# Performance work log

Hardware: AMD Instinct MI355X
Metric: run time of the kernel (lower is better)

The kernel has to match this reference:

```python
import jax, jax.numpy as jnp
import numpy as np

E = 8        # n_experts
K = 2        # top-k
DIM = 1024
HID = 2048   # swiglu hidden; fc1 out = 2*HID
B, T = 4, 2048


def setup_inputs() -> dict:
    key = jax.random.key(0)
    ks = jax.random.split(key, 7)
    s = 0.02
    return {
        "x": jax.random.normal(ks[0], (B, T, DIM), dtype=jnp.float32),
        "router_w": jax.random.normal(ks[1], (E, DIM), dtype=jnp.float32) * s,
        "router_b": jnp.zeros((E,), dtype=jnp.float32),
        "W1": jax.random.normal(ks[2], (E, DIM, 2 * HID), dtype=jnp.float32) * s,
        "b1": jnp.zeros((E, 2 * HID), dtype=jnp.float32),
        "W2": jax.random.normal(ks[3], (E, HID, DIM), dtype=jnp.float32) * s,
        "b2": jnp.zeros((E, DIM), dtype=jnp.float32),
    }


def _swiglu(h):
    h1, h2 = jnp.split(h, 2, axis=-1)
    return jax.nn.silu(h1) * h2


def reference(x, router_w, router_b, W1, b1, W2, b2):
    # Router: logits = Linear(dim, E), temperature = 1.0
    logits = jnp.einsum("btd,ed->bte", x, router_w) + router_b  # [B,T,E]
    topk_val, topk_idx = jax.lax.top_k(logits, K)               # [B,T,K]
    weights = jax.nn.softmax(topk_val, axis=-1)                 # softmax router
    # combine[b,t,e] = sum_k weights[b,t,k] * [topk_idx[b,t,k] == e]
    combine = jnp.sum(jax.nn.one_hot(topk_idx, E, dtype=x.dtype)
                      * weights[..., None], axis=-2)            # [B,T,E]
    out = jnp.zeros_like(x)
    # Fixed small loop over experts (structurally distinct weight slices).
    for e in range(E):
        h = jnp.einsum("btd,dh->bth", x, W1[e]) + b1[e]         # [B,T,2H]
        y = jnp.einsum("bth,hd->btd", _swiglu(h), W2[e]) + b2[e]
        out = out + combine[..., e:e + 1] * y
    return out
```

## Files before the change

### kernel.cpp

```cpp
#include <hip/hip_runtime.h>
#include <stdint.h>

typedef unsigned short u16;

#define E_    8
#define DIM_  1024
#define HID_  2048
#define H2_   4096
#define NTOK  8192

typedef __attribute__((ext_vector_type(8))) short bf16x8;
typedef __attribute__((ext_vector_type(4))) float f32x4;

__device__ __forceinline__ u16 f2bf(float f) {
  uint32_t u = __builtin_bit_cast(uint32_t, f);
  uint32_t r = (u + 0x7FFFu + ((u >> 16) & 1u)) >> 16;
  return (u16)r;
}
__device__ __forceinline__ float bf2f(u16 u) {
  return __builtin_bit_cast(float, (uint32_t)u << 16);
}

__device__ __forceinline__ void gload16(const void* g, void* l) {
  __builtin_amdgcn_global_load_lds(
      (const __attribute__((address_space(1))) void*)g,
      (__attribute__((address_space(3))) void*)l, 16, 0, 0);
}


__global__ void tconv(const float* __restrict__ src, u16* __restrict__ dst, int R, int C) {
  __shared__ float t[64][65];
  int e = blockIdx.z;
  int r0 = blockIdx.y * 64, c0 = blockIdx.x * 64;
  const float* s = src + (size_t)e * R * C;
  u16* d = dst + (size_t)e * R * C;
  int tid = threadIdx.x;
  int rr = tid >> 4, cc = (tid & 15) * 4;
#pragma unroll
  for (int p = 0; p < 4; ++p) {
    float4 v = *(const float4*)(s + (size_t)(r0 + p * 16 + rr) * C + c0 + cc);
    t[p * 16 + rr][cc + 0] = v.x; t[p * 16 + rr][cc + 1] = v.y;
    t[p * 16 + rr][cc + 2] = v.z; t[p * 16 + rr][cc + 3] = v.w;
  }
  __syncthreads();
  int cr = tid >> 3, rc = (tid & 7) * 8;
#pragma unroll
  for (int p = 0; p < 2; ++p) {
    union { u16 u[8]; uint4 v; } w;
#pragma unroll
    for (int j = 0; j < 8; ++j) w.u[j] = f2bf(t[rc + j][p * 32 + cr]);
    *(uint4*)(d + (size_t)(c0 + p * 32 + cr) * R + r0 + rc) = w.v;
  }
}


__global__ void routerA(const float* __restrict__ x, const float* __restrict__ rw,
                        const float* __restrict__ rb, u16* __restrict__ xb,
                        int* __restrict__ gcnt, int2* __restrict__ te_l,
                        float2* __restrict__ tw) {
  __shared__ float srw[E_ * DIM_];
  __shared__ float sb[E_];
  __shared__ int   hcnt[E_];

  int tid = threadIdx.x;
  for (int i = tid; i < E_ * DIM_ / 4; i += 256)
    ((float4*)srw)[i] = ((const float4*)rw)[i];
  if (tid < E_) { sb[tid] = rb[tid]; hcnt[tid] = 0; }
  __syncthreads();

  int wid = tid >> 6, lane = tid & 63;
#pragma unroll
  for (int s = 0; s < 2; ++s) {
    int t = blockIdx.x * 8 + wid * 2 + s;
    const float* xt = x + (size_t)t * DIM_;
    float acc[8] = {0.f, 0.f, 0.f, 0.f, 0.f, 0.f, 0.f, 0.f};
#pragma unroll
    for (int it = 0; it < 4; ++it) {
      int d = it * 256 + lane * 4;
      float4 xv = *(const float4*)(xt + d);
      ushort4 xo;
      xo.x = f2bf(xv.x); xo.y = f2bf(xv.y); xo.z = f2bf(xv.z); xo.w = f2bf(xv.w);
      *(ushort4*)(xb + (size_t)t * DIM_ + d) = xo;
#pragma unroll
      for (int e = 0; e < 8; ++e) {
        float4 rv = *(const float4*)(&srw[e * DIM_ + d]);
        acc[e] += xv.x * rv.x + xv.y * rv.y + xv.z * rv.z + xv.w * rv.w;
      }
    }
#pragma unroll
    for (int e = 0; e < 8; ++e)
#pragma unroll
      for (int off = 32; off; off >>= 1)
        acc[e] += __shfl_xor(acc[e], off, 64);
    if (lane == 0) {
      float v[8];
#pragma unroll
      for (int e = 0; e < 8; ++e) v[e] = acc[e] + sb[e];
      int i0 = 0;
#pragma unroll
      for (int e = 1; e < 8; ++e) if (v[e] > v[i0]) i0 = e;
      int i1 = (i0 == 0) ? 1 : 0;
#pragma unroll
      for (int e = 0; e < 8; ++e) if (e != i0 && v[e] > v[i1]) i1 = e;
      float w0 = 1.f / (1.f + expf(v[i1] - v[i0]));
      int l0 = atomicAdd(&hcnt[i0], 1);
      int l1 = atomicAdd(&hcnt[i1], 1);
      te_l[t] = make_int2((i0 << 8) | l0, (i1 << 8) | l1);
      tw[t] = make_float2(w0, 1.f - w0);
    }
  }
  __syncthreads();
  if (tid < E_) gcnt[tid * 1024 + blockIdx.x] = hcnt[tid];
}


__global__ void routerB(const int* __restrict__ gcnt, int* __restrict__ base_blk,
                        int* __restrict__ counts) {
  __shared__ int part[256];
  int tid = threadIdx.x;
#pragma unroll
  for (int e = 0; e < 8; ++e) {
    int4 v = *(const int4*)(gcnt + e * 1024 + tid * 4);
    int s = v.x + v.y + v.z + v.w;
    part[tid] = s;
    __syncthreads();
    for (int off = 1; off < 256; off <<= 1) {
      int o = (tid >= off) ? part[tid - off] : 0;
      __syncthreads();
      part[tid] += o;
      __syncthreads();
    }
    int ex = part[tid] - s;
    int tot = part[255];
    int4 b;
    b.x = ex; b.y = ex + v.x; b.z = ex + v.x + v.y; b.w = ex + v.x + v.y + v.z;
    *(int4*)(base_blk + e * 1024 + tid * 4) = b;
    if (tid == 0) counts[e] = tot;
    __syncthreads();
  }
}


__global__ void routerC(const int2* __restrict__ te_l, const float2* __restrict__ tw,
                        const int* __restrict__ base_blk, int* __restrict__ btok,
                        float* __restrict__ bw, int* __restrict__ tokrec) {
  int t = blockIdx.x * 256 + threadIdx.x;
  int2 r = te_l[t];
  float2 w = tw[t];
  int b = t >> 3;
  int e0 = r.x >> 8, l0 = r.x & 255;
  int e1 = r.y >> 8, l1 = r.y & 255;
  int p0 = base_blk[e0 * 1024 + b] + l0;
  int p1 = base_blk[e1 * 1024 + b] + l1;
  btok[e0 * NTOK + p0] = t; bw[e0 * NTOK + p0] = w.x; tokrec[t * 2 + 0] = (e0 << 13) | p0;
  btok[e1 * NTOK + p1] = t; bw[e1 * NTOK + p1] = w.y; tokrec[t * 2 + 1] = (e1 << 13) | p1;
}


__launch_bounds__(256, 4)
__global__ void gemm1(const u16* __restrict__ xb, const u16* __restrict__ w1t,
                      const float* __restrict__ b1, const int* __restrict__ counts,
                      const int* __restrict__ btok, u16* __restrict__ hb) {
  int e = blockIdx.z, mblk = blockIdx.y, nblk = blockIdx.x;
  int cnt = counts[e];
  if (mblk * 128 >= cnt) return;
  int base = 0;
#pragma unroll
  for (int i = 0; i < 8; ++i) base += (i < e) ? counts[i] : 0;

  __shared__ u16 lA[128 * 64];
  __shared__ u16 lB[128 * 64];
  __shared__ int sTok[128];

  int tid = threadIdx.x, wid = tid >> 6, lane = tid & 63;
  if (tid < 128) {
    int gr = mblk * 128 + tid;
    sTok[tid] = (gr < cnt) ? btok[e * NTOK + gr] : btok[e * NTOK];
  }
  __syncthreads();

  f32x4 acc[4][4] = {};
  int wr = wid >> 1, wc = wid & 1;
  int l15 = lane & 15, lhi = lane >> 4;
  const size_t w1e = (size_t)e * H2_ * DIM_;

  int segsw = ((lane & 7) ^ ((lane >> 3) & 7)) * 8;
  const u16* gA[4];
  const u16* gB[4];
#pragma unroll
  for (int i = 0; i < 4; ++i) {
    int r = wid * 32 + i * 8 + (lane >> 3);
    gA[i] = xb + (size_t)sTok[r] * DIM_ + segsw;
    int gcol = nblk * 64 + (r >> 6) * 32 + (r & 31) + ((r >> 5) & 1) * 2048;
    gB[i] = w1t + w1e + (size_t)gcol * DIM_ + segsw;
  }
  int rxor = (l15 & 7) * 8;

  for (int kt = 0; kt < DIM_ / 64; ++kt) {
#pragma unroll
    for (int i = 0; i < 4; ++i)
      gload16(gA[i] + kt * 64, &lA[(wid * 32 + i * 8) * 64]);
#pragma unroll
    for (int i = 0; i < 4; ++i)
      gload16(gB[i] + kt * 64, &lB[(wid * 32 + i * 8) * 64]);
    __syncthreads();
#pragma unroll
    for (int ks = 0; ks < 2; ++ks) {
      int segrd = ((ks * 4 + lhi) * 8) ^ rxor;
      bf16x8 a[4], b[4];
#pragma unroll
      for (int m = 0; m < 4; ++m)
        a[m] = *(const bf16x8*)&lA[(wr * 64 + m * 16 + l15) * 64 + segrd];
#pragma unroll
      for (int n = 0; n < 4; ++n)
        b[n] = *(const bf16x8*)&lB[(wc * 64 + n * 16 + l15) * 64 + segrd];
#pragma unroll
      for (int m = 0; m < 4; ++m)
#pragma unroll
        for (int n = 0; n < 4; ++n)
          acc[m][n] = __builtin_amdgcn_mfma_f32_16x16x32_bf16(a[m], b[n], acc[m][n], 0, 0, 0);
    }
    __syncthreads();
  }

#pragma unroll
  for (int n = 0; n < 2; ++n) {
    int outcol = nblk * 64 + wc * 32 + n * 16 + l15;
    float bb1 = b1[e * H2_ + outcol];
    float bb2 = b1[e * H2_ + outcol + HID_];
#pragma unroll
    for (int m = 0; m < 4; ++m) {
#pragma unroll
      for (int j = 0; j < 4; ++j) {
        int rt = wr * 64 + m * 16 + lhi * 4 + j;
        int gr = mblk * 128 + rt;
        if (gr < cnt) {
          float h1 = acc[m][n][j] + bb1;
          float h2 = acc[m][n + 2][j] + bb2;
          float s = (h1 / (1.f + __expf(-h1))) * h2;
          hb[(size_t)(base + gr) * HID_ + outcol] = f2bf(s);
        }
      }
    }
  }
}


__launch_bounds__(256, 4)
__global__ void gemm2(const u16* __restrict__ hb, const u16* __restrict__ w2t,
                      const float* __restrict__ b2, const int* __restrict__ counts,
                      const float* __restrict__ bw, u16* __restrict__ ybuf) {
  int e = blockIdx.z, mblk = blockIdx.y, nblk = blockIdx.x;
  int cnt = counts[e];
  if (mblk * 128 >= cnt) return;
  int base = 0;
#pragma unroll
  for (int i = 0; i < 8; ++i) base += (i < e) ? counts[i] : 0;

  __shared__ u16 lA[128 * 64];
  __shared__ u16 lB[128 * 64];
  __shared__ float sW[128];

  int tid = threadIdx.x, wid = tid >> 6, lane = tid & 63;
  if (tid < 128) {
    int gr = mblk * 128 + tid;
    sW[tid] = (gr < cnt) ? bw[e * NTOK + gr] : 0.f;
  }
  __syncthreads();

  f32x4 acc[4][4] = {};
  int wr = wid >> 1, wc = wid & 1;
  int l15 = lane & 15, lhi = lane >> 4;

  int segsw = ((lane & 7) ^ ((lane >> 3) & 7)) * 8;
  const u16* gA[4];
  const u16* gB[4];
#pragma unroll
  for (int i = 0; i < 4; ++i) {
    int r = wid * 32 + i * 8 + (lane >> 3);
    gA[i] = hb + (size_t)(base + mblk * 128 + r) * HID_ + segsw;
    gB[i] = w2t + (size_t)e * DIM_ * HID_ + (size_t)(nblk * 128 + r) * HID_ + segsw;
  }
  int rxor = (l15 & 7) * 8;

  for (int kt = 0; kt < HID_ / 64; ++kt) {
#pragma unroll
    for (int i = 0; i < 4; ++i) {
      gload16(gA[i] + kt * 64, &lA[(wid * 32 + i * 8) * 64]);
      gload16(gB[i] + kt * 64, &lB[(wid * 32 + i * 8) * 64]);
    }
    __syncthreads();
#pragma unroll
    for (int ks = 0; ks < 2; ++ks) {
      int segrd = ((ks * 4 + lhi) * 8) ^ rxor;
      bf16x8 a[4], b[4];
#pragma unroll
      for (int m = 0; m < 4; ++m)
        a[m] = *(const bf16x8*)&lA[(wr * 64 + m * 16 + l15) * 64 + segrd];
#pragma unroll
      for (int n = 0; n < 4; ++n)
        b[n] = *(const bf16x8*)&lB[(wc * 64 + n * 16 + l15) * 64 + segrd];
#pragma unroll
      for (int m = 0; m < 4; ++m)
#pragma unroll
        for (int n = 0; n < 4; ++n)
          acc[m][n] = __builtin_amdgcn_mfma_f32_16x16x32_bf16(a[m], b[n], acc[m][n], 0, 0, 0);
    }
    __syncthreads();
  }

#pragma unroll
  for (int n = 0; n < 4; ++n) {
    int col = nblk * 128 + wc * 64 + n * 16 + l15;
    float bb = b2[e * DIM_ + col];
#pragma unroll
    for (int m = 0; m < 4; ++m) {
#pragma unroll
      for (int j = 0; j < 4; ++j) {
        int rt = wr * 64 + m * 16 + lhi * 4 + j;
        int gr = mblk * 128 + rt;
        if (gr < cnt)
          ybuf[(size_t)(base + gr) * DIM_ + col] = f2bf(sW[rt] * (acc[m][n][j] + bb));
      }
    }
  }
}


__global__ void combine(const u16* __restrict__ ybuf, const int* __restrict__ tokrec,
                        const int* __restrict__ counts, float* __restrict__ out) {
  __shared__ int sbase[8];
  int tid = threadIdx.x;
  if (tid == 0) {
    int b = 0;
#pragma unroll
    for (int e = 0; e < 8; ++e) { sbase[e] = b; b += counts[e]; }
  }
  __syncthreads();
  int t = blockIdx.x;
  int r0 = tokrec[t * 2 + 0], r1 = tokrec[t * 2 + 1];
  size_t s0 = (size_t)(sbase[r0 >> 13] + (r0 & 8191)) * DIM_;
  size_t s1 = (size_t)(sbase[r1 >> 13] + (r1 & 8191)) * DIM_;
  int c = tid * 4;
  ushort4 a = *(const ushort4*)(ybuf + s0 + c);
  ushort4 b = *(const ushort4*)(ybuf + s1 + c);
  float4 o;
  o.x = bf2f(a.x) + bf2f(b.x);
  o.y = bf2f(a.y) + bf2f(b.y);
  o.z = bf2f(a.z) + bf2f(b.z);
  o.w = bf2f(a.w) + bf2f(b.w);
  *(float4*)(out + (size_t)t * DIM_ + c) = o;
}


extern "C" void kernel_launch(void* const* d_in, const int* in_sizes, int n_in,
                              void* d_out, int out_size, void* d_ws, size_t ws_size,
                              hipStream_t stream) {
  const float* x  = (const float*)d_in[0];
  const float* rw = (const float*)d_in[1];
  const float* rb = (const float*)d_in[2];
  const float* W1 = (const float*)d_in[3];
  const float* b1 = (const float*)d_in[4];
  const float* W2 = (const float*)d_in[5];
  const float* b2 = (const float*)d_in[6];
  float* out = (float*)d_out;

  char* ws = (char*)d_ws;
  int*    counts   = (int*)ws;
  int*    btok     = (int*)(ws + 256);
  float*  bw       = (float*)(ws + 256 + 262144);
  int*    tokrec   = (int*)(ws + 256 + 524288);
  int*    gcnt     = (int*)(ws + 655360);
  int*    base_blk = (int*)(ws + 688128);
  int2*   te_l     = (int2*)(ws + 720896);
  float2* tw       = (float2*)(ws + 786432);
  u16* xb  = (u16*)(ws + (1u << 20));
  u16* w1t = xb  + (size_t)NTOK * DIM_;
  u16* w2t = w1t + (size_t)E_ * H2_ * DIM_;
  u16* hb  = w2t + (size_t)E_ * DIM_ * HID_;
  u16* ybuf = w1t;

  tconv<<<dim3(H2_ / 64, DIM_ / 64, E_), 256, 0, stream>>>(W1, w1t, DIM_, H2_);
  tconv<<<dim3(DIM_ / 64, HID_ / 64, E_), 256, 0, stream>>>(W2, w2t, HID_, DIM_);
  routerA<<<1024, 256, 0, stream>>>(x, rw, rb, xb, gcnt, te_l, tw);
  routerB<<<1, 256, 0, stream>>>(gcnt, base_blk, counts);
  routerC<<<32, 256, 0, stream>>>(te_l, tw, base_blk, btok, bw, tokrec);

  gemm1<<<dim3(H2_ / 128, NTOK / 128, E_), 256, 0, stream>>>(xb, w1t, b1, counts, btok, hb);
  gemm2<<<dim3(DIM_ / 128, NTOK / 128, E_), 256, 0, stream>>>(hb, w2t, b2, counts, bw, ybuf);
  combine<<<NTOK, 256, 0, stream>>>(ybuf, tokrec, counts, out);
}
```

Measured before the change: 381.1 us.

## Split gemm2 K dimension in two, fuse weight conversions, widen combine

gemm2 now splits the HID reduction into two halves, each writing partial results to separate bf16 slabs. The combine kernel sums four partials per token, and each wave handles one token. The two weight-transpose kernels are merged into one launch. The intent is more gemm2 blocks for occupancy and less launch overhead, at the cost of extra ybuf traffic, an extra bf16 rounding on the partials, and a ybuf region reused inside w1t that must hold two slabs.

After: 375.9 us. About the same (-1.4%).

```diff
diff --git a/kernel.cpp b/kernel.cpp
--- a/kernel.cpp
+++ b/kernel.cpp
@@ -8,6 +8,7 @@
 #define HID_  2048
 #define H2_   4096
 #define NTOK  8192
+#define SLAB  ((size_t)NTOK * 2 * DIM_)
 
 typedef __attribute__((ext_vector_type(8))) short bf16x8;
 typedef __attribute__((ext_vector_type(4))) float f32x4;
@@ -28,10 +29,22 @@
 }
 
 
-__global__ void tconv(const float* __restrict__ src, u16* __restrict__ dst, int R, int C) {
+__global__ void tconvF(const float* __restrict__ W1, u16* __restrict__ w1t,
+                       const float* __restrict__ W2, u16* __restrict__ w2t) {
   __shared__ float t[64][65];
-  int e = blockIdx.z;
-  int r0 = blockIdx.y * 64, c0 = blockIdx.x * 64;
+  int b = blockIdx.x;
+  const float* src; u16* dst; int R, C, e, bx, by;
+  if (b < 8192) {
+    e = b >> 10; int rem = b & 1023;
+    bx = rem & 63; by = rem >> 6;
+    src = W1; dst = w1t; R = DIM_; C = H2_;
+  } else {
+    int b2 = b - 8192;
+    e = b2 >> 9; int rem = b2 & 511;
+    bx = rem & 15; by = rem >> 4;
+    src = W2; dst = w2t; R = HID_; C = DIM_;
+  }
+  int r0 = by * 64, c0 = bx * 64;
   const float* s = src + (size_t)e * R * C;
   u16* d = dst + (size_t)e * R * C;
   int tid = threadIdx.x;
@@ -250,7 +263,8 @@
 __global__ void gemm2(const u16* __restrict__ hb, const u16* __restrict__ w2t,
                       const float* __restrict__ b2, const int* __restrict__ counts,
                       const float* __restrict__ bw, u16* __restrict__ ybuf) {
-  int e = blockIdx.z, mblk = blockIdx.y, nblk = blockIdx.x;
+  int e = blockIdx.z, mblk = blockIdx.y;
+  int nblk = blockIdx.x & 7, khalf = blockIdx.x >> 3;
   int cnt = counts[e];
   if (mblk * 128 >= cnt) return;
   int base = 0;
@@ -273,17 +287,18 @@
   int l15 = lane & 15, lhi = lane >> 4;
 
   int segsw = ((lane & 7) ^ ((lane >> 3) & 7)) * 8;
+  int koff = khalf * (HID_ / 2);
   const u16* gA[4];
   const u16* gB[4];
 #pragma unroll
   for (int i = 0; i < 4; ++i) {
     int r = wid * 32 + i * 8 + (lane >> 3);
-    gA[i] = hb + (size_t)(base + mblk * 128 + r) * HID_ + segsw;
-    gB[i] = w2t + (size_t)e * DIM_ * HID_ + (size_t)(nblk * 128 + r) * HID_ + segsw;
+    gA[i] = hb + (size_t)(base + mblk * 128 + r) * HID_ + koff + segsw;
+    gB[i] = w2t + (size_t)e * DIM_ * HID_ + (size_t)(nblk * 128 + r) * HID_ + koff + segsw;
   }
   int rxor = (l15 & 7) * 8;
 
-  for (int kt = 0; kt < HID_ / 64; ++kt) {
+  for (int kt = 0; kt < HID_ / 128; ++kt) {
 #pragma unroll
     for (int i = 0; i < 4; ++i) {
       gload16(gA[i] + kt * 64, &lA[(wid * 32 + i * 8) * 64]);
@@ -309,10 +324,11 @@
     __syncthreads();
   }
 
+  u16* yb = ybuf + (size_t)khalf * SLAB;
 #pragma unroll
   for (int n = 0; n < 4; ++n) {
     int col = nblk * 128 + wc * 64 + n * 16 + l15;
-    float bb = b2[e * DIM_ + col];
+    float bb = (khalf == 0) ? b2[e * DIM_ + col] : 0.f;
 #pragma unroll
     for (int m = 0; m < 4; ++m) {
 #pragma unroll
@@ -320,7 +336,7 @@
         int rt = wr * 64 + m * 16 + lhi * 4 + j;
         int gr = mblk * 128 + rt;
         if (gr < cnt)
-          ybuf[(size_t)(base + gr) * DIM_ + col] = f2bf(sW[rt] * (acc[m][n][j] + bb));
+          yb[(size_t)(base + gr) * DIM_ + col] = f2bf(sW[rt] * (acc[m][n][j] + bb));
       }
     }
   }
@@ -331,25 +347,31 @@
                         const int* __restrict__ counts, float* __restrict__ out) {
   __shared__ int sbase[8];
   int tid = threadIdx.x;
-  if (tid == 0) {
+  if (tid < 8) {
     int b = 0;
 #pragma unroll
-    for (int e = 0; e < 8; ++e) { sbase[e] = b; b += counts[e]; }
-  }
-  __syncthreads();
-  int t = blockIdx.x;
+    for (int e = 0; e < 8; ++e) { if (e == tid) sbase[e] = b; b += counts[e]; }
+  }
+  __syncthreads();
+  int wid = tid >> 6, lane = tid & 63;
+  int t = blockIdx.x * 4 + wid;
   int r0 = tokrec[t * 2 + 0], r1 = tokrec[t * 2 + 1];
   size_t s0 = (size_t)(sbase[r0 >> 13] + (r0 & 8191)) * DIM_;
   size_t s1 = (size_t)(sbase[r1 >> 13] + (r1 & 8191)) * DIM_;
-  int c = tid * 4;
-  ushort4 a = *(const ushort4*)(ybuf + s0 + c);
-  ushort4 b = *(const ushort4*)(ybuf + s1 + c);
-  float4 o;
-  o.x = bf2f(a.x) + bf2f(b.x);
-  o.y = bf2f(a.y) + bf2f(b.y);
-  o.z = bf2f(a.z) + bf2f(b.z);
-  o.w = bf2f(a.w) + bf2f(b.w);
-  *(float4*)(out + (size_t)t * DIM_ + c) = o;
+#pragma unroll
+  for (int p = 0; p < 4; ++p) {
+    int c = (lane + p * 64) * 4;
+    ushort4 a0 = *(const ushort4*)(ybuf + s0 + c);
+    ushort4 a1 = *(const ushort4*)(ybuf + SLAB + s0 + c);
+    ushort4 b0 = *(const ushort4*)(ybuf + s1 + c);
+    ushort4 b1 = *(const ushort4*)(ybuf + SLAB + s1 + c);
+    float4 o;
+    o.x = bf2f(a0.x) + bf2f(a1.x) + bf2f(b0.x) + bf2f(b1.x);
+    o.y = bf2f(a0.y) + bf2f(a1.y) + bf2f(b0.y) + bf2f(b1.y);
+    o.z = bf2f(a0.z) + bf2f(a1.z) + bf2f(b0.z) + bf2f(b1.z);
+    o.w = bf2f(a0.w) + bf2f(a1.w) + bf2f(b0.w) + bf2f(b1.w);
+    *(float4*)(out + (size_t)t * DIM_ + c) = o;
+  }
 }
 
 
@@ -380,13 +402,12 @@
   u16* hb  = w2t + (size_t)E_ * DIM_ * HID_;
   u16* ybuf = w1t;
 
-  tconv<<<dim3(H2_ / 64, DIM_ / 64, E_), 256, 0, stream>>>(W1, w1t, DIM_, H2_);
-  tconv<<<dim3(DIM_ / 64, HID_ / 64, E_), 256, 0, stream>>>(W2, w2t, HID_, DIM_);
+  tconvF<<<12288, 256, 0, stream>>>(W1, w1t, W2, w2t);
   routerA<<<1024, 256, 0, stream>>>(x, rw, rb, xb, gcnt, te_l, tw);
   routerB<<<1, 256, 0, stream>>>(gcnt, base_blk, counts);
   routerC<<<32, 256, 0, stream>>>(te_l, tw, base_blk, btok, bw, tokrec);
 
   gemm1<<<dim3(H2_ / 128, NTOK / 128, E_), 256, 0, stream>>>(xb, w1t, b1, counts, btok, hb);
-  gemm2<<<dim3(DIM_ / 128, NTOK / 128, E_), 256, 0, stream>>>(hb, w2t, b2, counts, bw, ybuf);
-  combine<<<NTOK, 256, 0, stream>>>(ybuf, tokrec, counts, out);
-}
+  gemm2<<<dim3(16, NTOK / 128, E_), 256, 0, stream>>>(hb, w2t, b2, counts, bw, ybuf);
+  combine<<<NTOK / 4, 256, 0, stream>>>(ybuf, tokrec, counts, out);
+}
```
